# Kernel tuning notes

Hardware: AMD Instinct MI355X
Metric: run time of the kernel (lower is better)

Reference implementation:

```python
import jax, jax.numpy as jnp
import numpy as np
from jax import lax

BETA = 0.5        # Sinkhron beta
N_ITER = 20       # got_iteration
THRESH = 0.1      # P > 0.1 threshold
NL_I = 5          # apply_non_linearity(..., 'elu', i=5)
EPS = 1e-9


def setup_inputs() -> dict:
    key = jax.random.key(0)
    k1, k2 = jax.random.split(key)
    B, N, D = 128, 512, 128
    h = jax.random.normal(k1, (B, N, D), dtype=jnp.float32)
    W0 = jnp.ones((D,), dtype=jnp.float32)
    W1 = jnp.ones((D,), dtype=jnp.float32)
    lengths = jax.random.randint(k2, (B,), 0, N, dtype=jnp.int32)
    return {"h": h, "W0": W0, "W1": W1, "lengths": lengths}


def _forward(h, W0, W1, lengths):
    B, N, D = h.shape
    lengths = jnp.maximum(lengths, 1)
    mask = (jnp.arange(N)[None, :] < lengths[:, None])          # [B, N] bool
    mf = mask.astype(h.dtype)
    mask2 = mf[:, :, None] * mf[:, None, :]                      # [B, N, N]

    # internal_forward: Diag layers with relu between (mlp_act='relu')
    h = h * W0
    h = jax.nn.relu(h)
    h = h * W1

    # cost_matrix_batch_torch: cosine similarity, add identity diag, mask
    hn = h / (jnp.linalg.norm(h, axis=-1, keepdims=True) + 1e-12)
    sim = jnp.einsum('bnd,bmd->bnm', hn, hn)                     # [B, N, N]
    sim = sim + jnp.eye(N, dtype=h.dtype)                        # add_eye_diag
    sim = sim * mask2
    cost = (1.0 - sim) * mask2

    # Sinkhorn with uniform marginals on valid nodes, fixed iterations
    n = lengths.astype(h.dtype)
    mu = mf / n[:, None]                                         # [B, N]
    K = jnp.exp(-cost / BETA) * mask2                            # [B, N, N]

    def body(carry, _):
        u, v = carry
        u = mu / (jnp.einsum('bnm,bm->bn', K, v) + EPS) * mf
        v = mu / (jnp.einsum('bnm,bn->bm', K, u) + EPS) * mf
        return (u, v), None

    (u, v), _ = lax.scan(body, (mf, mf), None, length=N_ITER)
    P = u[:, :, None] * K * v[:, None, :]                        # transport plan

    # P.detach(); scale by number of nodes per graph; threshold
    P = lax.stop_gradient(P)
    P = n[:, None, None] * P
    A = (P > THRESH).astype(h.dtype)
    similarity = A * sim
    # apply_non_linearity 'elu': elu(x*i - i) + 1
    out = jax.nn.elu(similarity * NL_I - NL_I) + 1.0
    return out


def reference(h, W0, W1, lengths):
    return _forward(h, W0, W1, lengths)
```

## Files before the change

### kernel.cpp

```cpp
#include <hip/hip_runtime.h>

#define BB 128
#define NN 512
#define DD 128
#define SLOT_STRIDE 544

__global__ __launch_bounds__(256) void hn_kernel(const float* __restrict__ h,
                                                 const float* __restrict__ W0,
                                                 const float* __restrict__ W1,
                                                 float* __restrict__ hn) {
    int wave = (int)((blockIdx.x * blockDim.x + threadIdx.x) >> 6);
    int lane = threadIdx.x & 63;
    const float2* h2 = (const float2*)(h + (size_t)wave * DD);
    float2 w0 = ((const float2*)W0)[lane];
    float2 w1 = ((const float2*)W1)[lane];
    float2 x = h2[lane];
    float p0 = fmaxf(x.x * w0.x, 0.0f) * w1.x;
    float p1 = fmaxf(x.y * w0.y, 0.0f) * w1.y;
    float ss = p0 * p0 + p1 * p1;
#pragma unroll
    for (int m = 32; m; m >>= 1) ss += __shfl_xor(ss, m);
    float inv = 1.0f / (sqrtf(ss) + 1e-12f);
    float2 o;
    o.x = p0 * inv;
    o.y = p1 * inv;
    ((float2*)(hn + (size_t)wave * DD))[lane] = o;
}

#define KC 32
__global__ __launch_bounds__(256) void sim_kernel(const float* __restrict__ hn,
                                                  const int* __restrict__ lengths,
                                                  float* __restrict__ K) {
    __shared__ float As[KC][132];
    __shared__ float Bs[KC][132];
    __shared__ int pre[BB + 1];
    int tid = threadIdx.x;
    if (tid == 0) {
        int acc = 0;
        for (int b = 0; b < BB; b++) {
            pre[b] = acc;
            int len = max(lengths[b], 1);
            int nt = (len + 127) >> 7;
            acc += nt * nt;
        }
        pre[BB] = acc;
    }
    __syncthreads();
    int total = pre[BB];

    int lr = tid >> 3;
    int lk = (tid & 7) << 2;
    int tx = tid & 15, ty = tid >> 4;

    for (int t = blockIdx.x; t < total; t += gridDim.x) {
        int lo = 0, hi = BB;
        while (lo + 1 < hi) {
            int mid = (lo + hi) >> 1;
            if (pre[mid] <= t) lo = mid; else hi = mid;
        }
        int b = lo;
        int local = t - pre[b];
        int len = max(lengths[b], 1);
        int nt = (len + 127) >> 7;
        int ti = local / nt;
        int tj = local - ti * nt;
        int r0 = ti << 7, c0 = tj << 7;
        const float* base = hn + (size_t)b * NN * DD;
        float acc[8][8] = {};

        for (int kc = 0; kc < DD; kc += KC) {
#pragma unroll
            for (int rr = 0; rr < 128; rr += 32) {
                float4 a = *(const float4*)(base + (size_t)(r0 + lr + rr) * DD + kc + lk);
                As[lk + 0][lr + rr] = a.x; As[lk + 1][lr + rr] = a.y;
                As[lk + 2][lr + rr] = a.z; As[lk + 3][lr + rr] = a.w;
                float4 bb = *(const float4*)(base + (size_t)(c0 + lr + rr) * DD + kc + lk);
                Bs[lk + 0][lr + rr] = bb.x; Bs[lk + 1][lr + rr] = bb.y;
                Bs[lk + 2][lr + rr] = bb.z; Bs[lk + 3][lr + rr] = bb.w;
            }
            __syncthreads();
#pragma unroll
            for (int kk = 0; kk < KC; kk++) {
                float4 a0 = *(const float4*)&As[kk][ty * 8];
                float4 a1 = *(const float4*)&As[kk][ty * 8 + 4];
                float4 b0 = *(const float4*)&Bs[kk][tx * 4];
                float4 b1 = *(const float4*)&Bs[kk][64 + tx * 4];
                float ar[8] = {a0.x, a0.y, a0.z, a0.w, a1.x, a1.y, a1.z, a1.w};
                float bc[8] = {b0.x, b0.y, b0.z, b0.w, b1.x, b1.y, b1.z, b1.w};
#pragma unroll
                for (int r = 0; r < 8; r++)
#pragma unroll
                    for (int c = 0; c < 8; c++)
                        acc[r][c] = fmaf(ar[r], bc[c], acc[r][c]);
            }
            __syncthreads();
        }
        float* out = K + (size_t)b * NN * NN;
#pragma unroll
        for (int r = 0; r < 8; r++) {
            int i = r0 + ty * 8 + r;
            if (i >= len) continue;
#pragma unroll
            for (int cg = 0; cg < 2; cg++) {
                int j0 = c0 + cg * 64 + tx * 4;
                if (j0 >= len) continue;
                float vv[4];
#pragma unroll
                for (int c = 0; c < 4; c++) {
                    float s = acc[r][cg * 4 + c] + ((i == j0 + c) ? 1.0f : 0.0f);
                    vv[c] = expf(2.0f * s - 2.0f);
                }
                float4 o;
                o.x = vv[0]; o.y = vv[1]; o.z = vv[2]; o.w = vv[3];
                *(float4*)(out + (size_t)i * NN + j0) = o;
            }
        }
    }
}

__device__ __forceinline__ float dot8(float4 A, float4 B, float4 x0, float4 x1) {
    float d = fmaf(A.x, x0.x, fmaf(A.y, x0.y, fmaf(A.z, x0.z, A.w * x0.w)));
    return fmaf(B.x, x1.x, fmaf(B.y, x1.y, fmaf(B.z, x1.z, fmaf(B.w, x1.w, d))));
}

__global__ __launch_bounds__(512, 4) void coop_sink(const float* __restrict__ K,
                                                    float* __restrict__ u_buf,
                                                    float* __restrict__ v_buf,
                                                    const int* __restrict__ lengths,
                                                    float* __restrict__ slots) {
    __shared__ float xb[NN];
    __shared__ float pv[8 * NN];
    __shared__ int Sh[16], Pre[16];

    int g = blockIdx.x;
    int x = g & 7;
    int j = g >> 3;
    int tid = threadIdx.x;

    if (tid == 0) {
        long long w[16]; long long W = 0;
        for (int m = 0; m < 16; m++) {
            long long L = max(lengths[x + 8 * m], 1);
            w[m] = L * L; W += w[m];
        }
        int t_[16]; int used = 0;
        for (int m = 0; m < 16; m++) { t_[m] = (int)((48LL * w[m]) / W); used += t_[m]; }
        int R = 48 - used;
        bool bump[16] = {};
        for (int r = 0; r < R; r++) {
            int best = 0; long long bestrem = -1;
            for (int m = 0; m < 16; m++) {
                if (bump[m]) continue;
                long long rem = 48LL * w[m] - (long long)t_[m] * W;
                if (rem > bestrem) { bestrem = rem; best = m; }
            }
            bump[best] = true; t_[best]++;
        }
        int acc = 0;
        for (int m = 0; m < 16; m++) {
            int S = 1 + t_[m]; if (S > 16) S = 16;
            Pre[m] = acc; Sh[m] = S; acc += S;
        }
    }
    __syncthreads();

    int m = -1;
    for (int mm = 0; mm < 16; mm++)
        if (j >= Pre[mm] && j < Pre[mm] + Sh[mm]) { m = mm; break; }
    if (m < 0) return;
    int b = x + 8 * m;
    int q = j - Pre[m];
    int S = Sh[m];
    int jbase = Pre[m];

    int len = max(lengths[b], 1);
    int len4 = (len + 3) & ~3;
    int rpq = (len + S - 1) / S;
    int r_lo = q * rpq;
    int nrows = min(len - r_lo, rpq);
    if (nrows < 0) nrows = 0;
    float inv_n = 1.0f / (float)len;

    int w = tid >> 6, l = tid & 63;
    int c0 = 4 * l, c1 = 256 + 4 * l;
    bool a0 = c0 < len4, a1 = c1 < len4;
    const float* Kb = K + (size_t)b * NN * NN;

    xb[tid] = (tid < len) ? 1.0f : 0.0f;
    __syncthreads();

    for (int t = 0; t < 20; t++) {
        float4 xv0 = *(const float4*)(xb + c0);
        float4 xv1 = *(const float4*)(xb + c1);
        float4 pa = {0, 0, 0, 0}, pb = {0, 0, 0, 0};

        int i = w;
#pragma unroll 2
        for (; i + 24 < nrows; i += 32) {
            const float* g0 = Kb + (size_t)(r_lo + i) * NN;
            const float* g1 = g0 + (size_t)8 * NN;
            const float* g2 = g0 + (size_t)16 * NN;
            const float* g3 = g0 + (size_t)24 * NN;
            float4 A0 = {0,0,0,0}, A1 = {0,0,0,0}, A2 = {0,0,0,0}, A3 = {0,0,0,0};
            float4 B0 = {0,0,0,0}, B1 = {0,0,0,0}, B2 = {0,0,0,0}, B3 = {0,0,0,0};
            if (a0) {
                A0 = *(const float4*)(g0 + c0); A1 = *(const float4*)(g1 + c0);
                A2 = *(const float4*)(g2 + c0); A3 = *(const float4*)(g3 + c0);
            }
            if (a1) {
                B0 = *(const float4*)(g0 + c1); B1 = *(const float4*)(g1 + c1);
                B2 = *(const float4*)(g2 + c1); B3 = *(const float4*)(g3 + c1);
            }
            float d0 = dot8(A0, B0, xv0, xv1);
            float d1 = dot8(A1, B1, xv0, xv1);
            float d2 = dot8(A2, B2, xv0, xv1);
            float d3 = dot8(A3, B3, xv0, xv1);
#pragma unroll
            for (int mm = 32; mm; mm >>= 1) {
                d0 += __shfl_xor(d0, mm);
                d1 += __shfl_xor(d1, mm);
                d2 += __shfl_xor(d2, mm);
                d3 += __shfl_xor(d3, mm);
            }
            float u0 = inv_n / (d0 + 1e-9f), u1 = inv_n / (d1 + 1e-9f);
            float u2 = inv_n / (d2 + 1e-9f), u3 = inv_n / (d3 + 1e-9f);
            pa.x = fmaf(A0.x, u0, fmaf(A1.x, u1, fmaf(A2.x, u2, fmaf(A3.x, u3, pa.x))));
            pa.y = fmaf(A0.y, u0, fmaf(A1.y, u1, fmaf(A2.y, u2, fmaf(A3.y, u3, pa.y))));
            pa.z = fmaf(A0.z, u0, fmaf(A1.z, u1, fmaf(A2.z, u2, fmaf(A3.z, u3, pa.z))));
            pa.w = fmaf(A0.w, u0, fmaf(A1.w, u1, fmaf(A2.w, u2, fmaf(A3.w, u3, pa.w))));
            pb.x = fmaf(B0.x, u0, fmaf(B1.x, u1, fmaf(B2.x, u2, fmaf(B3.x, u3, pb.x))));
            pb.y = fmaf(B0.y, u0, fmaf(B1.y, u1, fmaf(B2.y, u2, fmaf(B3.y, u3, pb.y))));
            pb.z = fmaf(B0.z, u0, fmaf(B1.z, u1, fmaf(B2.z, u2, fmaf(B3.z, u3, pb.z))));
            pb.w = fmaf(B0.w, u0, fmaf(B1.w, u1, fmaf(B2.w, u2, fmaf(B3.w, u3, pb.w))));
            if (t == 19 && l == 0) {
                float* ub = u_buf + (size_t)b * NN + r_lo;
                ub[i] = u0; ub[i + 8] = u1; ub[i + 16] = u2; ub[i + 24] = u3;
            }
        }
        for (; i < nrows; i += 8) {
            const float* g0 = Kb + (size_t)(r_lo + i) * NN;
            float4 A = {0,0,0,0}, B = {0,0,0,0};
            if (a0) A = *(const float4*)(g0 + c0);
            if (a1) B = *(const float4*)(g0 + c1);
            float d = dot8(A, B, xv0, xv1);
#pragma unroll
            for (int mm = 32; mm; mm >>= 1) d += __shfl_xor(d, mm);
            float uu = inv_n / (d + 1e-9f);
            pa.x = fmaf(A.x, uu, pa.x); pa.y = fmaf(A.y, uu, pa.y);
            pa.z = fmaf(A.z, uu, pa.z); pa.w = fmaf(A.w, uu, pa.w);
            pb.x = fmaf(B.x, uu, pb.x); pb.y = fmaf(B.y, uu, pb.y);
            pb.z = fmaf(B.z, uu, pb.z); pb.w = fmaf(B.w, uu, pb.w);
            if (t == 19 && l == 0) u_buf[(size_t)b * NN + r_lo + i] = uu;
        }

        *(float4*)(pv + w * NN + c0) = pa;
        *(float4*)(pv + w * NN + c1) = pb;
        __syncthreads();
        float* slotp = slots + ((size_t)(t & 1) * 512 + g) * SLOT_STRIDE;
        int c = tid;
        float s0 = pv[c] + pv[NN + c] + pv[2 * NN + c] + pv[3 * NN + c] +
                   pv[4 * NN + c] + pv[5 * NN + c] + pv[6 * NN + c] + pv[7 * NN + c];
        __hip_atomic_store(slotp + c, s0, __ATOMIC_RELAXED, __HIP_MEMORY_SCOPE_AGENT);
        asm volatile("s_waitcnt vmcnt(0)" ::: "memory");
        __syncthreads();
        if (tid == 0)
            __hip_atomic_store((int*)(slotp + 512), t + 1, __ATOMIC_RELAXED,
                               __HIP_MEMORY_SCOPE_AGENT);
        if (tid < S && tid != q) {
            const int* tagp = (const int*)(slots +
                ((size_t)(t & 1) * 512 + (size_t)(x + 8 * (jbase + tid))) * SLOT_STRIDE + 512);
            while (__hip_atomic_load(tagp, __ATOMIC_RELAXED, __HIP_MEMORY_SCOPE_AGENT) != t + 1)
                __builtin_amdgcn_s_sleep(1);
        }
        __syncthreads();

        const float* sbase = slots + ((size_t)(t & 1) * 512) * SLOT_STRIDE;
        float t0 = s0;
        for (int s = 1; s < S; s++) {
            int k = q + s; if (k >= S) k -= S;
            t0 += __hip_atomic_load(sbase + (size_t)(x + 8 * (jbase + k)) * SLOT_STRIDE + c,
                                    __ATOMIC_RELAXED, __HIP_MEMORY_SCOPE_AGENT);
        }
        float v0 = (c < len) ? (inv_n / (t0 + 1e-9f)) : 0.0f;
        if (t < 19) {
            xb[c] = v0;
        } else if (c >= r_lo && c < r_lo + nrows) {
            v_buf[(size_t)b * NN + c] = v0;
        }
        __syncthreads();
    }
}

__global__ __launch_bounds__(256) void epi_kernel(float* __restrict__ io,
                                                  const float* __restrict__ u,
                                                  const float* __restrict__ v,
                                                  const int* __restrict__ lengths) {
    const float E5 = 0.006737946999085467f;
    size_t idx = (size_t)blockIdx.x * 256 + threadIdx.x;
    int b = (int)(idx >> 16);
    int r = (int)(idx >> 7) & (NN - 1);
    int c4 = ((int)idx & 127) << 2;
    int len = max(lengths[b], 1);
    float4 o;
    if (r >= len || c4 >= len) {
        o.x = E5; o.y = E5; o.z = E5; o.w = E5;
        ((float4*)io)[idx] = o;
        return;
    }
    float4 k = ((float4*)io)[idx];
    float ui = u[(size_t)b * NN + r];
    float4 vv = *(const float4*)(v + (size_t)b * NN + c4);
    float t = (float)len * ui;
    float kv[4] = {k.x, k.y, k.z, k.w};
    float vj[4] = {vv.x, vv.y, vv.z, vv.w};
    float ov[4];
#pragma unroll
    for (int c = 0; c < 4; c++) {
        float Kc = kv[c];
        float P = t * Kc * vj[c];
        bool valid = (c4 + c) < len;
        if (valid && P > 0.1f) {
            float x = 2.5f * logf(Kc);
            ov[c] = (x > 0.0f) ? (x + 1.0f) : expf(x);
        } else {
            ov[c] = E5;
        }
    }
    o.x = ov[0]; o.y = ov[1]; o.z = ov[2]; o.w = ov[3];
    ((float4*)io)[idx] = o;
}

extern "C" void kernel_launch(void* const* d_in, const int* in_sizes, int n_in,
                              void* d_out, int out_size, void* d_ws, size_t ws_size,
                              hipStream_t stream) {
    const float* h = (const float*)d_in[0];
    const float* W0 = (const float*)d_in[1];
    const float* W1 = (const float*)d_in[2];
    const int* lengths = (const int*)d_in[3];
    float* K = (float*)d_out;

    char* ws = (char*)d_ws;
    float* hn = (float*)ws;
    size_t off = (size_t)BB * NN * DD * 4;
    float* u = (float*)(ws + off);     off += (size_t)BB * NN * 4;
    float* v = (float*)(ws + off);     off += (size_t)BB * NN * 4;
    float* slots = (float*)(ws + off); off += (size_t)2 * 512 * SLOT_STRIDE * 4;

    hn_kernel<<<BB * NN / 4, 256, 0, stream>>>(h, W0, W1, hn);
    sim_kernel<<<1024, 256, 0, stream>>>(hn, lengths, K);

    coop_sink<<<512, 512, 0, stream>>>(K, u, v, lengths, slots);

    epi_kernel<<<(unsigned)((size_t)BB * NN * NN / 4 / 256), 256, 0, stream>>>(K, u, v, lengths);
}
```

Before: 411.0 us.

## Cache first 64 K rows per block in registers across Sinkhorn iterations

```diff
diff --git a/kernel.cpp b/kernel.cpp
--- a/kernel.cpp
+++ b/kernel.cpp
@@ -138,29 +138,20 @@
     int tid = threadIdx.x;
 
     if (tid == 0) {
-        long long w[16]; long long W = 0;
+        int need[16]; int ssum = 0;
         for (int m = 0; m < 16; m++) {
-            long long L = max(lengths[x + 8 * m], 1);
-            w[m] = L * L; W += w[m];
-        }
-        int t_[16]; int used = 0;
-        for (int m = 0; m < 16; m++) { t_[m] = (int)((48LL * w[m]) / W); used += t_[m]; }
-        int R = 48 - used;
-        bool bump[16] = {};
-        for (int r = 0; r < R; r++) {
-            int best = 0; long long bestrem = -1;
-            for (int m = 0; m < 16; m++) {
-                if (bump[m]) continue;
-                long long rem = 48LL * w[m] - (long long)t_[m] * W;
-                if (rem > bestrem) { bestrem = rem; best = m; }
-            }
-            bump[best] = true; t_[best]++;
+            int L = max(lengths[x + 8 * m], 1);
+            need[m] = (L + 63) >> 6;
+            ssum += need[m];
+        }
+        while (ssum > 64) {
+            int best = 0, bv = need[0];
+            for (int m = 1; m < 16; m++)
+                if (need[m] > bv) { bv = need[m]; best = m; }
+            need[best]--; ssum--;
         }
         int acc = 0;
-        for (int m = 0; m < 16; m++) {
-            int S = 1 + t_[m]; if (S > 16) S = 16;
-            Pre[m] = acc; Sh[m] = S; acc += S;
-        }
+        for (int m = 0; m < 16; m++) { Pre[m] = acc; Sh[m] = need[m]; acc += need[m]; }
     }
     __syncthreads();
 
@@ -186,6 +177,8 @@
     bool a0 = c0 < len4, a1 = c1 < len4;
     const float* Kb = K + (size_t)b * NN * NN;
 
+    float4 kA[8], kB[8];
+
     xb[tid] = (tid < len) ? 1.0f : 0.0f;
     __syncthreads();
 
@@ -194,52 +187,46 @@
         float4 xv1 = *(const float4*)(xb + c1);
         float4 pa = {0, 0, 0, 0}, pb = {0, 0, 0, 0};
 
-        int i = w;
-#pragma unroll 2
-        for (; i + 24 < nrows; i += 32) {
+        if (t == 0) {
+#pragma unroll
+            for (int o = 0; o < 8; o++) {
+                int i = w + 8 * o;
+                float4 z = {0, 0, 0, 0};
+                kA[o] = z; kB[o] = z;
+                bool rv = i < nrows;
+                const float* g0 = Kb + (size_t)(r_lo + i) * NN;
+                if (rv && a0) kA[o] = *(const float4*)(g0 + c0);
+                if (rv && a1) kB[o] = *(const float4*)(g0 + c1);
+            }
+        }
+
+        float dd[8], uu_[8];
+#pragma unroll
+        for (int o = 0; o < 8; o++) dd[o] = dot8(kA[o], kB[o], xv0, xv1);
+#pragma unroll
+        for (int mm = 32; mm; mm >>= 1) {
+#pragma unroll
+            for (int o = 0; o < 8; o++) dd[o] += __shfl_xor(dd[o], mm);
+        }
+#pragma unroll
+        for (int o = 0; o < 8; o++) uu_[o] = inv_n / (dd[o] + 1e-9f);
+#pragma unroll
+        for (int o = 0; o < 8; o++) {
+            pa.x = fmaf(kA[o].x, uu_[o], pa.x); pa.y = fmaf(kA[o].y, uu_[o], pa.y);
+            pa.z = fmaf(kA[o].z, uu_[o], pa.z); pa.w = fmaf(kA[o].w, uu_[o], pa.w);
+            pb.x = fmaf(kB[o].x, uu_[o], pb.x); pb.y = fmaf(kB[o].y, uu_[o], pb.y);
+            pb.z = fmaf(kB[o].z, uu_[o], pb.z); pb.w = fmaf(kB[o].w, uu_[o], pb.w);
+        }
+        if (t == 19 && l == 0) {
+#pragma unroll
+            for (int o = 0; o < 8; o++)
+                if (w + 8 * o < nrows)
+                    u_buf[(size_t)b * NN + r_lo + w + 8 * o] = uu_[o];
+        }
+
+        for (int i = 64 + w; i < nrows; i += 8) {
             const float* g0 = Kb + (size_t)(r_lo + i) * NN;
-            const float* g1 = g0 + (size_t)8 * NN;
-            const float* g2 = g0 + (size_t)16 * NN;
-            const float* g3 = g0 + (size_t)24 * NN;
-            float4 A0 = {0,0,0,0}, A1 = {0,0,0,0}, A2 = {0,0,0,0}, A3 = {0,0,0,0};
-            float4 B0 = {0,0,0,0}, B1 = {0,0,0,0}, B2 = {0,0,0,0}, B3 = {0,0,0,0};
-            if (a0) {
-                A0 = *(const float4*)(g0 + c0); A1 = *(const float4*)(g1 + c0);
-                A2 = *(const float4*)(g2 + c0); A3 = *(const float4*)(g3 + c0);
-            }
-            if (a1) {
-                B0 = *(const float4*)(g0 + c1); B1 = *(const float4*)(g1 + c1);
-                B2 = *(const float4*)(g2 + c1); B3 = *(const float4*)(g3 + c1);
-            }
-            float d0 = dot8(A0, B0, xv0, xv1);
-            float d1 = dot8(A1, B1, xv0, xv1);
-            float d2 = dot8(A2, B2, xv0, xv1);
-            float d3 = dot8(A3, B3, xv0, xv1);
-#pragma unroll
-            for (int mm = 32; mm; mm >>= 1) {
-                d0 += __shfl_xor(d0, mm);
-                d1 += __shfl_xor(d1, mm);
-                d2 += __shfl_xor(d2, mm);
-                d3 += __shfl_xor(d3, mm);
-            }
-            float u0 = inv_n / (d0 + 1e-9f), u1 = inv_n / (d1 + 1e-9f);
-            float u2 = inv_n / (d2 + 1e-9f), u3 = inv_n / (d3 + 1e-9f);
-            pa.x = fmaf(A0.x, u0, fmaf(A1.x, u1, fmaf(A2.x, u2, fmaf(A3.x, u3, pa.x))));
-            pa.y = fmaf(A0.y, u0, fmaf(A1.y, u1, fmaf(A2.y, u2, fmaf(A3.y, u3, pa.y))));
-            pa.z = fmaf(A0.z, u0, fmaf(A1.z, u1, fmaf(A2.z, u2, fmaf(A3.z, u3, pa.z))));
-            pa.w = fmaf(A0.w, u0, fmaf(A1.w, u1, fmaf(A2.w, u2, fmaf(A3.w, u3, pa.w))));
-            pb.x = fmaf(B0.x, u0, fmaf(B1.x, u1, fmaf(B2.x, u2, fmaf(B3.x, u3, pb.x))));
-            pb.y = fmaf(B0.y, u0, fmaf(B1.y, u1, fmaf(B2.y, u2, fmaf(B3.y, u3, pb.y))));
-            pb.z = fmaf(B0.z, u0, fmaf(B1.z, u1, fmaf(B2.z, u2, fmaf(B3.z, u3, pb.z))));
-            pb.w = fmaf(B0.w, u0, fmaf(B1.w, u1, fmaf(B2.w, u2, fmaf(B3.w, u3, pb.w))));
-            if (t == 19 && l == 0) {
-                float* ub = u_buf + (size_t)b * NN + r_lo;
-                ub[i] = u0; ub[i + 8] = u1; ub[i + 16] = u2; ub[i + 24] = u3;
-            }
-        }
-        for (; i < nrows; i += 8) {
-            const float* g0 = Kb + (size_t)(r_lo + i) * NN;
-            float4 A = {0,0,0,0}, B = {0,0,0,0};
+            float4 A = {0, 0, 0, 0}, B = {0, 0, 0, 0};
             if (a0) A = *(const float4*)(g0 + c0);
             if (a1) B = *(const float4*)(g0 + c1);
             float d = dot8(A, B, xv0, xv1);
```

After: 399.3 us. 1.03x faster.
